# Optimization experiments

Hardware: AMD Instinct MI355X
Metric: run time of the kernel (lower is better)

## Reference

```python
import jax, jax.numpy as jnp
import numpy as np
from jax import lax

B, C, H, W = 4, 4, 64, 64
NREF = 16
DECAY = 0.8
MAX_DELAY = 24
WET_MIX, FEEDBACK, ROOM = 0.3, 0.4, 0.5  # module defaults (static Python floats)
HEADS = 4  # min(4, channels)


def _conv2d(x, w, b, pad, groups=1):
    y = lax.conv_general_dilated(x, w, (1, 1), [(pad, pad), (pad, pad)],
                                 dimension_numbers=('NCHW', 'OIHW', 'NCHW'),
                                 feature_group_count=groups)
    return y if b is None else y + b[None, :, None, None]


def _fade(n, fw=4):
    f = np.ones(n, np.float32)
    f[:fw] = np.linspace(0.6, 1.0, fw)
    f[-fw:] = np.linspace(1.0, 0.6, fw)
    return jnp.asarray(f)


def _delay_line(x, delay, yf, xf):
    # torch: shifts=(int(delay*1), int(delay*2)) on dims (2,3); delay>0 so int==floor
    ys = jnp.floor(delay).astype(jnp.int32)
    xs = jnp.floor(delay * 2.0).astype(jnp.int32)
    s = jnp.roll(x, shift=(ys, xs), axis=(2, 3))
    # shifts are always nonzero here (scaled delays >= 6), so both fades apply
    return s * yf[None, None, :, None] * xf[None, None, None, :]


def setup_inputs() -> dict:
    key = jax.random.key(0)
    ks = jax.random.split(key, 16)
    n = jax.random.normal
    return {
        'x': n(ks[0], (B, C, H, W), jnp.float32),
        'reflection_weights': n(ks[1], (NREF,), jnp.float32) * 0.1,
        'reflection_delays': jax.random.randint(ks[2], (NREF,), 1, MAX_DELAY).astype(jnp.float32),
        'diffusion_strength': n(ks[3], (NREF,), jnp.float32) * 0.2,
        'spatial_w': n(ks[4], (2 * C, C, 3, 3), jnp.float32) * 0.1,
        'spatial_b': jnp.zeros((2 * C,), jnp.float32),
        'feedback_w': n(ks[5], (C, C, 3, 3), jnp.float32) * 0.1,
        'feedback_b': jnp.zeros((C,), jnp.float32),
        'damp1_w': n(ks[6], (C // 2, C, 1, 1), jnp.float32) * 0.3,
        'damp1_b': jnp.zeros((C // 2,), jnp.float32),
        'damp2_w': n(ks[7], (C, C // 2, 1, 1), jnp.float32) * 0.3,
        'damp2_b': jnp.zeros((C,), jnp.float32),
        'attn_in_w': n(ks[8], (3 * C, C), jnp.float32) * 0.3,
        'attn_in_b': jnp.zeros((3 * C,), jnp.float32),
        'attn_out_w': n(ks[9], (C, C), jnp.float32) * 0.3,
        'attn_out_b': jnp.zeros((C,), jnp.float32),
        'out_w': n(ks[10], (C, 3 * C, 1, 1), jnp.float32) * 0.2,
        'out_b': jnp.zeros((C,), jnp.float32),
    }


def reference(x, reflection_weights, reflection_delays, diffusion_strength,
              spatial_w, spatial_b, feedback_w, feedback_b,
              damp1_w, damp1_b, damp2_w, damp2_b,
              attn_in_w, attn_in_b, attn_out_w, attn_out_b, out_w, out_b):
    b, c, h, w = x.shape
    rsf = 8.0 / NREF  # reflection_scale_factor = 0.5
    scaled_delays = reflection_delays * ROOM * 12.0 * rsf
    wet = jnp.zeros_like(x)
    fb = x * 0.1
    spatial_features = _conv2d(x, spatial_w, spatial_b, 1)
    yf, xf = _fade(h), _fade(w)
    feedback_scale = 1.0 + rsf * 0.5
    for i in range(NREF):
        delay = scaled_delays[i]
        weight = jax.nn.sigmoid(reflection_weights[i]) * (DECAY ** i) * (1.0 + FEEDBACK * feedback_scale)
        r = _delay_line(fb, delay, yf, xf)
        r = _conv2d(r, feedback_w, feedback_b, 1)
        damping = jax.nn.sigmoid(
            _conv2d(jax.nn.silu(_conv2d(r, damp1_w, damp1_b, 0)), damp2_w, damp2_b, 0))
        r = r * damping
        wet = wet + r * weight * (4.0 * rsf)
        fb = fb + r * (FEEDBACK * 1.2 * rsf)
        if FEEDBACK > 0.3 and i > 0:
            prev = _delay_line(fb, delay * 0.5, yf, xf)
            fb = fb + prev * (FEEDBACK * 0.4 * rsf)
    # spatial self-attention over flattened pixels (embed=4, 4 heads, head_dim=1)
    S = h * w
    hd = c // HEADS
    wf = wet.reshape(b, c, S).transpose(0, 2, 1)  # [b, S, c]
    qkv = wf @ attn_in_w.T + attn_in_b
    q, k, v = jnp.split(qkv, 3, axis=-1)
    def split_heads(t):
        return t.reshape(b, S, HEADS, hd).transpose(0, 2, 1, 3)  # [b, H, S, hd]
    q, k, v = split_heads(q), split_heads(k), split_heads(v)
    scores = jnp.einsum('bhqd,bhkd->bhqk', q, k) / jnp.sqrt(jnp.float32(hd))
    attn = jax.nn.softmax(scores, axis=-1)
    o = jnp.einsum('bhqk,bhkd->bhqd', attn, v).transpose(0, 2, 1, 3).reshape(b, S, c)
    o = o @ attn_out_w.T + attn_out_b
    wet = o.transpose(0, 2, 1).reshape(b, c, h, w)
    # ROOM=0.5 > 0.3 -> box blur, kernel = max(3, int(0.5*3*0.5)) = 3
    kb = 3
    blur_k = jnp.ones((c, 1, kb, kb), jnp.float32) / (kb * kb)
    wet = _conv2d(wet, blur_k, None, kb // 2, groups=c)
    # FEEDBACK=0.4 > 0.2 -> edge enhancement
    ek = jnp.array([[-1., -1., -1.], [-1., 8., -1.], [-1., -1., -1.]], jnp.float32)
    edge_k = jnp.tile(ek[None, None], (c, 1, 1, 1))
    edge = _conv2d(wet, edge_k, None, 1, groups=c)
    wet = wet + edge * (FEEDBACK * 0.2 * rsf)
    # ROOM=0.5 <= 0.8 -> no contrast adjustment
    combined = jnp.concatenate([spatial_features, wet], axis=1)
    processed = _conv2d(combined, out_w, out_b, 0)
    return x * (1.0 - WET_MIX) + processed * WET_MIX
```

## Files before the change

### kernel.cpp

```cpp
#include <hip/hip_runtime.h>

#define LOG2E 1.4426950408889634f
#define RNB 32

typedef float v2f __attribute__((ext_vector_type(2)));

__device__ __forceinline__ float fsig(float z) {
    return __builtin_amdgcn_rcpf(1.0f + exp2f(-z * LOG2E));
}

__device__ __forceinline__ float4 ld_fb(const unsigned long long* p) {
    unsigned long long a = __hip_atomic_load(p,     __ATOMIC_RELAXED, __HIP_MEMORY_SCOPE_AGENT);
    unsigned long long b = __hip_atomic_load(p + 1, __ATOMIC_RELAXED, __HIP_MEMORY_SCOPE_AGENT);
    float2 lo = __builtin_bit_cast(float2, a);
    float2 hi = __builtin_bit_cast(float2, b);
    return make_float4(lo.x, lo.y, hi.x, hi.y);
}

__device__ __forceinline__ void st_fb(unsigned long long* p, float4 v) {
    __hip_atomic_store(p,     __builtin_bit_cast(unsigned long long, make_float2(v.x, v.y)),
                       __ATOMIC_RELAXED, __HIP_MEMORY_SCOPE_AGENT);
    __hip_atomic_store(p + 1, __builtin_bit_cast(unsigned long long, make_float2(v.z, v.w)),
                       __ATOMIC_RELAXED, __HIP_MEMORY_SCOPE_AGENT);
}

__global__ __launch_bounds__(256) void bar_init(unsigned* cnt) {
    for (int j = threadIdx.x; j < 1024; j += 256) cnt[j] = 0u;
}

__device__ __forceinline__ void conv_damp_l(
    const float4* __restrict__ src, int yq, int xq, int ys, int xs,
    const float* fe, const float4 wr[9][4],
    const float4 d1w0, const float4 d1w1, const float2 d1b, const float4 d2p[4],
    float rv[4])
{
    float r[4] = { d2p[0].w, d2p[1].w, d2p[2].w, d2p[3].w };
    #pragma unroll
    for (int a = 0; a < 3; ++a) {
        int yy = yq - 1 + a;
        float fy = fe[yy + 1];
        const float4* rowp = src + (((yy - ys) & 63) << 6);
        #pragma unroll
        for (int qq = 0; qq < 3; ++qq) {
            int xt = xq - 1 + qq;
            float f = fy * fe[xt + 1];
            float4 v = rowp[(xt - xs) & 63];
            float s0 = v.x * f, s1 = v.y * f, s2 = v.z * f, s3 = v.w * f;
            #pragma unroll
            for (int co = 0; co < 4; ++co) {
                float4 w = wr[a * 3 + qq][co];
                r[co] = fmaf(w.x, s0, fmaf(w.y, s1, fmaf(w.z, s2, fmaf(w.w, s3, r[co]))));
            }
        }
    }
    float z0 = fmaf(d1w0.x, r[0], fmaf(d1w0.y, r[1], fmaf(d1w0.z, r[2], fmaf(d1w0.w, r[3], d1b.x))));
    float z1 = fmaf(d1w1.x, r[0], fmaf(d1w1.y, r[1], fmaf(d1w1.z, r[2], fmaf(d1w1.w, r[3], d1b.y))));
    float h0 = z0 * fsig(z0);
    float h1 = z1 * fsig(z1);
    #pragma unroll
    for (int c = 0; c < 4; ++c) {
        float dm = fsig(fmaf(d2p[c].x, h0, fmaf(d2p[c].y, h1, d2p[c].z)));
        rv[c] = r[c] * dm;
    }
}

__global__ __launch_bounds__(512) void reverb_mb(
    const float* __restrict__ x, const float* __restrict__ rw, const float* __restrict__ dl,
    const float* __restrict__ fbw, const float* __restrict__ fbb,
    const float* __restrict__ d1wg, const float* __restrict__ d1bg,
    const float* __restrict__ d2wg, const float* __restrict__ d2bg,
    unsigned long long* __restrict__ GA, unsigned long long* __restrict__ GB,
    unsigned* __restrict__ cnt, float4* __restrict__ ws_wet)
{
    __shared__ float4 fbL[4096];
    __shared__ float fe[66];
    __shared__ float4 wvsL[36];
    __shared__ float s_rw[16], s_dl[16];
    __shared__ float4 s_mlp[7];

    const int tid = threadIdx.x;
    const int b   = blockIdx.x >> 3;
    const int blk = blockIdx.x & 7;

    if (tid < 66) {
        float f = 0.0f;
        if (tid >= 1 && tid <= 64) {
            int j = tid - 1;
            f = 1.0f;
            if (j < 4) f = 0.6f + (0.4f / 3.0f) * j;
            else if (j >= 60) f = 0.6f + (0.4f / 3.0f) * (63 - j);
        }
        fe[tid] = f;
    }
    if (tid >= 128 && tid < 164) {
        int t2 = tid - 128, n = t2 >> 2, co = t2 & 3;
        wvsL[t2] = make_float4(fbw[(co * 4 + 0) * 9 + n], fbw[(co * 4 + 1) * 9 + n],
                               fbw[(co * 4 + 2) * 9 + n], fbw[(co * 4 + 3) * 9 + n]);
    }
    if (tid >= 192 && tid < 208) s_rw[tid - 192] = rw[tid - 192];
    if (tid >= 256 && tid < 272) s_dl[tid - 256] = dl[tid - 256];
    if (tid == 320) {
        s_mlp[0] = make_float4(d1wg[0], d1wg[1], d1wg[2], d1wg[3]);
        s_mlp[1] = make_float4(d1wg[4], d1wg[5], d1wg[6], d1wg[7]);
        s_mlp[2] = make_float4(d1bg[0], d1bg[1], 0.0f, 0.0f);
        for (int c = 0; c < 4; ++c)
            s_mlp[3 + c] = make_float4(d2wg[c * 2], d2wg[c * 2 + 1], d2bg[c], fbb[c]);
    }
    for (int s = tid; s < 4096; s += 512) {
        float4 v;
        v.x = 0.1f * x[((b * 4 + 0) << 12) + s];
        v.y = 0.1f * x[((b * 4 + 1) << 12) + s];
        v.z = 0.1f * x[((b * 4 + 2) << 12) + s];
        v.w = 0.1f * x[((b * 4 + 3) << 12) + s];
        fbL[s] = v;
    }
    __syncthreads();

    float4 wr[9][4];
    #pragma unroll
    for (int n = 0; n < 9; ++n)
        #pragma unroll
        for (int co = 0; co < 4; ++co) wr[n][co] = wvsL[n * 4 + co];
    const float4 d1w0 = s_mlp[0], d1w1 = s_mlp[1];
    const float2 d1b = make_float2(s_mlp[2].x, s_mlp[2].y);
    float4 d2p[4] = { s_mlp[3], s_mlp[4], s_mlp[5], s_mlp[6] };

    const int ly = tid >> 6;
    const int y0 = (blk << 3) + ly;
    const int xx = tid & 63;
    float4 fbv = fbL[(y0 << 6) + xx];

    unsigned long long* Ab = GA + (b << 13);
    unsigned long long* Bb = GB + (b << 13);
    unsigned* cb = cnt + b * 240;

    float acc0 = 0.0f, acc1 = 0.0f, acc2 = 0.0f, acc3 = 0.0f;
    float decay = 1.0f;
    #pragma unroll 1
    for (int i = 0; i < 16; ++i) {
        float d = s_dl[i];
        int ys  = ((int)(3.0f * d)) & 63;
        int xs  = ((int)(6.0f * d)) & 63;
        float wgt = fsig(s_rw[i]) * decay * 3.0f;

        float rv[4];
        conv_damp_l(fbL, y0, xx, ys, xs, fe, wr, d1w0, d1w1, d1b, d2p, rv);
        acc0 = fmaf(rv[0], wgt, acc0);
        acc1 = fmaf(rv[1], wgt, acc1);
        acc2 = fmaf(rv[2], wgt, acc2);
        acc3 = fmaf(rv[3], wgt, acc3);
        float4 g = make_float4(fbv.x + 0.24f * rv[0], fbv.y + 0.24f * rv[1],
                               fbv.z + 0.24f * rv[2], fbv.w + 0.24f * rv[3]);
        if (i == 15) break;

        unsigned long long* G = (i & 1) ? Bb : Ab;
        st_fb(G + (((y0 << 6) + xx) << 1), g);

        __syncthreads();
        if (tid == 0) {
            if (__hip_atomic_fetch_add(&cb[i * 16], 1u, __ATOMIC_RELAXED,
                                       __HIP_MEMORY_SCOPE_AGENT) + 1u < 8u) {
                while (__hip_atomic_load(&cb[i * 16], __ATOMIC_RELAXED,
                                         __HIP_MEMORY_SCOPE_AGENT) < 8u)
                    __builtin_amdgcn_s_sleep(1);
            }
        }
        __syncthreads();

        int ys2 = ((int)(1.5f * d)) & 63;
        int xs2 = ((int)(3.0f * d)) & 63;
        float dn = s_dl[i + 1];
        int ysn = ((int)(3.0f * dn)) & 63;

        if (i > 0) {
            int yr = (y0 - ys2) & 63, xr = (xx - xs2) & 63;
            float4 g2 = ld_fb(G + (((yr << 6) + xr) << 1));
            float f = 0.08f * fe[y0 + 1] * fe[xx + 1];
            fbv = make_float4(fmaf(f, g2.x, g.x), fmaf(f, g2.y, g.y),
                              fmaf(f, g2.z, g.z), fmaf(f, g2.w, g.w));
        } else {
            fbv = g;
        }

        #pragma unroll
        for (int rpt = 0; rpt < 2; ++rpt) {
            int idx = tid + (rpt << 9);
            if (idx < 640) {
                int j  = idx >> 6, xc = idx & 63;
                int rr = ((blk << 3) - 1 + j - ysn) & 63;
                float4 g1 = ld_fb(G + (((rr << 6) + xc) << 1));
                float4 nv = g1;
                if (i > 0) {
                    int r2 = (rr - ys2) & 63, x2 = (xc - xs2) & 63;
                    float4 g2 = ld_fb(G + (((r2 << 6) + x2) << 1));
                    float f = 0.08f * fe[rr + 1] * fe[xc + 1];
                    nv = make_float4(fmaf(f, g2.x, g1.x), fmaf(f, g2.y, g1.y),
                                     fmaf(f, g2.z, g1.z), fmaf(f, g2.w, g1.w));
                }
                fbL[(rr << 6) + xc] = nv;
            }
        }
        __syncthreads();
        decay *= 0.8f;
    }

    ws_wet[(b << 12) + (y0 << 6) + xx] = make_float4(acc0, acc1, acc2, acc3);
}

__global__ __launch_bounds__(512) void attn_kernel(
    const float4* __restrict__ wet, const float* __restrict__ aiw,
    const float* __restrict__ aib, float* __restrict__ o_out)
{
    __shared__ float ksf[4096];
    __shared__ float vsf[4096];
    __shared__ float redmx[8], redmn[8];
    __shared__ float2 part[2048];

    const int tid = threadIdx.x;
    const int bid = blockIdx.x;
    const int b  = bid >> 7;
    const int h  = (bid >> 5) & 3;
    const int qc = bid & 31;

    float wq[4], wk[4], wv[4];
    #pragma unroll
    for (int c = 0; c < 4; ++c) {
        wq[c] = aiw[h * 4 + c];
        wk[c] = aiw[(4 + h) * 4 + c];
        wv[c] = aiw[(8 + h) * 4 + c];
    }
    const float bq = aib[h], bk = aib[4 + h], bv = aib[8 + h];

    float lmax = -1e30f, lmin = 1e30f;
    for (int s = tid; s < 4096; s += 512) {
        float4 w4 = wet[(b << 12) + s];
        float k = wk[0] * w4.x + wk[1] * w4.y + wk[2] * w4.z + wk[3] * w4.w + bk;
        float v = wv[0] * w4.x + wv[1] * w4.y + wv[2] * w4.z + wv[3] * w4.w + bv;
        ksf[s] = k; vsf[s] = v;
        lmax = fmaxf(lmax, k); lmin = fminf(lmin, k);
    }
    #pragma unroll
    for (int off = 32; off > 0; off >>= 1) {
        lmax = fmaxf(lmax, __shfl_xor(lmax, off));
        lmin = fminf(lmin, __shfl_xor(lmin, off));
    }
    if ((tid & 63) == 0) { redmx[tid >> 6] = lmax; redmn[tid >> 6] = lmin; }
    __syncthreads();
    float kmax = redmx[0], kmin = redmn[0];
    #pragma unroll
    for (int w = 1; w < 8; ++w) { kmax = fmaxf(kmax, redmx[w]); kmin = fminf(kmin, redmn[w]); }

    const int rs = tid & 31;
    const int kg = tid >> 5;
    v2f qL2[4], nmL2[4];
    #pragma unroll
    for (int rr = 0; rr < 4; ++rr) {
        int row = (qc << 7) + (rs << 2) + rr;
        float4 w4 = wet[(b << 12) + row];
        float q = wq[0] * w4.x + wq[1] * w4.y + wq[2] * w4.z + wq[3] * w4.w + bq;
        float m = (q >= 0.0f) ? q * kmax : q * kmin;
        float qL = q * LOG2E, mL = m * LOG2E;
        qL2[rr] = (v2f){qL, qL}; nmL2[rr] = (v2f){-mL, -mL};
    }

    const v2f* ks2 = (const v2f*)ksf;
    const v2f* vs2 = (const v2f*)vsf;
    v2f den2[4], num2[4];
    #pragma unroll
    for (int rr = 0; rr < 4; ++rr) { den2[rr] = (v2f){0.f, 0.f}; num2[rr] = (v2f){0.f, 0.f}; }

    const int j0 = kg << 6;
    #pragma unroll 4
    for (int j = j0 * 2; j < j0 * 2 + 128; ++j) {
        v2f kk = ks2[j];
        v2f vv = vs2[j];
        #pragma unroll
        for (int rr = 0; rr < 4; ++rr) {
            v2f arg = __builtin_elementwise_fma(qL2[rr], kk, nmL2[rr]);
            v2f e;
            e.x = __builtin_amdgcn_exp2f(arg.x);
            e.y = __builtin_amdgcn_exp2f(arg.y);
            den2[rr] += e;
            num2[rr] = __builtin_elementwise_fma(e, vv, num2[rr]);
        }
    }
    #pragma unroll
    for (int rr = 0; rr < 4; ++rr)
        part[(kg << 7) + (rs << 2) + rr] =
            make_float2(den2[rr].x + den2[rr].y, num2[rr].x + num2[rr].y);
    __syncthreads();
    if (tid < 128) {
        float dd = 0.0f, nn = 0.0f;
        #pragma unroll
        for (int g = 0; g < 16; ++g) {
            float2 p = part[(g << 7) + tid];
            dd += p.x; nn += p.y;
        }
        int row = (qc << 7) + tid;
        o_out[((b << 12) + row) * 4 + h] = nn * __builtin_amdgcn_rcpf(dd);
    }
}

__global__ __launch_bounds__(256) void projblur_kernel(
    const float4* __restrict__ o_in, const float* __restrict__ aow,
    const float* __restrict__ aob, float* __restrict__ blur)
{
    __shared__ float wetL[4096];
    const int tid = threadIdx.x;
    const int bc = blockIdx.x;
    const int b = bc >> 2, c = bc & 3;
    const float w0 = aow[c * 4], w1 = aow[c * 4 + 1], w2 = aow[c * 4 + 2], w3 = aow[c * 4 + 3];
    const float bb = aob[c];
    for (int s = tid; s < 4096; s += 256) {
        float4 o = o_in[(b << 12) + s];
        wetL[s] = w0 * o.x + w1 * o.y + w2 * o.z + w3 * o.w + bb;
    }
    __syncthreads();
    for (int s = tid; s < 4096; s += 256) {
        int y = s >> 6, x = s & 63;
        float acc = 0.0f;
        for (int dy = -1; dy <= 1; ++dy) {
            int yy = y + dy; if (yy < 0 || yy > 63) continue;
            for (int dx = -1; dx <= 1; ++dx) {
                int xx = x + dx; if (xx < 0 || xx > 63) continue;
                acc += wetL[yy * 64 + xx];
            }
        }
        blur[(bc << 12) + s] = acc * (1.0f / 9.0f);
    }
}

__global__ __launch_bounds__(256) void final_kernel(
    const float* __restrict__ x, const float* __restrict__ sw, const float* __restrict__ sb,
    const float* __restrict__ ow, const float* __restrict__ ob,
    const float* __restrict__ blur, float* __restrict__ out)
{
    __shared__ float s_sw[288], s_ow[48], s_sb[8], s_ob[4];
    int tid = threadIdx.x;
    for (int j = tid; j < 288; j += 256) s_sw[j] = sw[j];
    if (tid < 48) s_ow[tid] = ow[tid];
    if (tid < 8) s_sb[tid] = sb[tid];
    if (tid < 4) s_ob[tid] = ob[tid];
    __syncthreads();

    int t = blockIdx.x * 256 + tid;
    int b = t >> 12, s = t & 4095;
    int y = s >> 6, xx0 = s & 63;

    float spat[8];
    #pragma unroll
    for (int co = 0; co < 8; ++co) spat[co] = s_sb[co];
    for (int dy = -1; dy <= 1; ++dy) {
        int yy = y + dy;
        if (yy < 0 || yy > 63) continue;
        for (int dx = -1; dx <= 1; ++dx) {
            int xc = xx0 + dx;
            if (xc < 0 || xc > 63) continue;
            int ky = dy + 1, kx = dx + 1;
            #pragma unroll
            for (int ci = 0; ci < 4; ++ci) {
                float xv = x[((b * 4 + ci) << 12) + yy * 64 + xc];
                #pragma unroll
                for (int co = 0; co < 8; ++co)
                    spat[co] += s_sw[((co * 4 + ci) * 3 + ky) * 3 + kx] * xv;
            }
        }
    }

    float wetF[4];
    #pragma unroll
    for (int c = 0; c < 4; ++c) {
        const float* pl = blur + ((b * 4 + c) << 12);
        float center = pl[s];
        float sum9 = 0.0f;
        for (int dy = -1; dy <= 1; ++dy) {
            int yy = y + dy;
            if (yy < 0 || yy > 63) continue;
            for (int dx = -1; dx <= 1; ++dx) {
                int xc = xx0 + dx;
                if (xc < 0 || xc > 63) continue;
                sum9 += pl[yy * 64 + xc];
            }
        }
        float edge = 9.0f * center - sum9;
        wetF[c] = center + 0.04f * edge;
    }

    #pragma unroll
    for (int co = 0; co < 4; ++co) {
        float p = s_ob[co];
        #pragma unroll
        for (int j = 0; j < 8; ++j) p += s_ow[co * 12 + j] * spat[j];
        #pragma unroll
        for (int c = 0; c < 4; ++c) p += s_ow[co * 12 + 8 + c] * wetF[c];
        float xc = x[((b * 4 + co) << 12) + s];
        out[((b * 4 + co) << 12) + s] = 0.7f * xc + 0.3f * p;
    }
}

extern "C" void kernel_launch(void* const* d_in, const int* in_sizes, int n_in,
                              void* d_out, int out_size, void* d_ws, size_t ws_size,
                              hipStream_t stream)
{
    (void)in_sizes; (void)n_in; (void)out_size; (void)ws_size;
    const float* x    = (const float*)d_in[0];
    const float* rw   = (const float*)d_in[1];
    const float* dl   = (const float*)d_in[2];
    const float* sw   = (const float*)d_in[4];
    const float* sb   = (const float*)d_in[5];
    const float* fbw  = (const float*)d_in[6];
    const float* fbb  = (const float*)d_in[7];
    const float* d1w  = (const float*)d_in[8];
    const float* d1b  = (const float*)d_in[9];
    const float* d2w  = (const float*)d_in[10];
    const float* d2b  = (const float*)d_in[11];
    const float* aiw  = (const float*)d_in[12];
    const float* aib  = (const float*)d_in[13];
    const float* aow  = (const float*)d_in[14];
    const float* aob  = (const float*)d_in[15];
    const float* ow   = (const float*)d_in[16];
    const float* ob   = (const float*)d_in[17];
    float* out = (float*)d_out;

    float* ws_wet  = (float*)d_ws;
    float* GA      = ws_wet + 65536;
    float* GB      = GA + 65536;
    unsigned* cnt  = (unsigned*)(GB + 65536);
    float* ws_o    = GA;
    float* ws_blur = GB;

    bar_init<<<1, 256, 0, stream>>>(cnt);
    reverb_mb<<<RNB, 512, 0, stream>>>(x, rw, dl, fbw, fbb, d1w, d1b, d2w, d2b,
                                       (unsigned long long*)GA, (unsigned long long*)GB,
                                       cnt, (float4*)ws_wet);
    attn_kernel<<<512, 512, 0, stream>>>((const float4*)ws_wet, aiw, aib, ws_o);
    projblur_kernel<<<16, 256, 0, stream>>>((const float4*)ws_o, aow, aob, ws_blur);
    final_kernel<<<64, 256, 0, stream>>>(x, sw, sb, ow, ob, ws_blur, out);
}
```

Before: 186.6 us.

## Replace counter barrier with per-block epoch flags and split projblur into bands

The inter-block barrier in the reverb kernel changes from one atomic counter per iteration, which thread 0 increments and spins on, to per-block epoch flags. Each block publishes its iteration number and then polls the minimum of the 8 flags for its batch, which removes the atomic RMW and one __syncthreads. Separately, projblur is split into 4 row bands per (b,c) with a halo, giving 64 blocks instead of 16 for more parallelism. The cost is that every thread now spins on global loads, and the halo rows are recomputed by neighbouring bands.

After: 188.8 us. About the same (+1.2%).

```diff
diff --git a/kernel.cpp b/kernel.cpp
--- a/kernel.cpp
+++ b/kernel.cpp
@@ -132,7 +132,7 @@
 
     unsigned long long* Ab = GA + (b << 13);
     unsigned long long* Bb = GB + (b << 13);
-    unsigned* cb = cnt + b * 240;
+    unsigned* flg = cnt + b * 16;
 
     float acc0 = 0.0f, acc1 = 0.0f, acc2 = 0.0f, acc3 = 0.0f;
     float decay = 1.0f;
@@ -157,15 +157,23 @@
         st_fb(G + (((y0 << 6) + xx) << 1), g);
 
         __syncthreads();
-        if (tid == 0) {
-            if (__hip_atomic_fetch_add(&cb[i * 16], 1u, __ATOMIC_RELAXED,
-                                       __HIP_MEMORY_SCOPE_AGENT) + 1u < 8u) {
-                while (__hip_atomic_load(&cb[i * 16], __ATOMIC_RELAXED,
-                                         __HIP_MEMORY_SCOPE_AGENT) < 8u)
-                    __builtin_amdgcn_s_sleep(1);
-            }
-        }
-        __syncthreads();
+        if (tid == 0)
+            __hip_atomic_store(&flg[blk], (unsigned)(i + 1),
+                               __ATOMIC_RELAXED, __HIP_MEMORY_SCOPE_AGENT);
+        {
+            const unsigned tgt = (unsigned)(i + 1);
+            for (;;) {
+                unsigned mn = 0xFFFFFFFFu;
+                #pragma unroll
+                for (int k = 0; k < 8; ++k) {
+                    unsigned fv = __hip_atomic_load(&flg[k], __ATOMIC_RELAXED,
+                                                    __HIP_MEMORY_SCOPE_AGENT);
+                    mn = (fv < mn) ? fv : mn;
+                }
+                if (mn >= tgt) break;
+                __builtin_amdgcn_s_sleep(1);
+            }
+        }
 
         int ys2 = ((int)(1.5f * d)) & 63;
         int xs2 = ((int)(3.0f * d)) & 63;
@@ -305,28 +313,39 @@
     const float4* __restrict__ o_in, const float* __restrict__ aow,
     const float* __restrict__ aob, float* __restrict__ blur)
 {
-    __shared__ float wetL[4096];
-    const int tid = threadIdx.x;
-    const int bc = blockIdx.x;
+    __shared__ float wetL[18 * 64];
+    const int tid  = threadIdx.x;
+    const int bc   = blockIdx.x >> 2;
+    const int band = blockIdx.x & 3;
     const int b = bc >> 2, c = bc & 3;
+    const int y0 = band << 4;
     const float w0 = aow[c * 4], w1 = aow[c * 4 + 1], w2 = aow[c * 4 + 2], w3 = aow[c * 4 + 3];
     const float bb = aob[c];
-    for (int s = tid; s < 4096; s += 256) {
-        float4 o = o_in[(b << 12) + s];
-        wetL[s] = w0 * o.x + w1 * o.y + w2 * o.z + w3 * o.w + bb;
+
+    {
+        const int xx = tid & 63;
+        for (int lr = tid >> 6; lr < 18; lr += 4) {
+            int gy = y0 - 1 + lr;
+            if (gy >= 0 && gy < 64) {
+                float4 o = o_in[(b << 12) + (gy << 6) + xx];
+                wetL[lr * 64 + xx] = w0 * o.x + w1 * o.y + w2 * o.z + w3 * o.w + bb;
+            }
+        }
     }
     __syncthreads();
-    for (int s = tid; s < 4096; s += 256) {
-        int y = s >> 6, x = s & 63;
+    for (int s = tid; s < 1024; s += 256) {
+        int ly = s >> 6, x = s & 63;
+        int gy = y0 + ly;
         float acc = 0.0f;
         for (int dy = -1; dy <= 1; ++dy) {
-            int yy = y + dy; if (yy < 0 || yy > 63) continue;
+            int yy = gy + dy; if (yy < 0 || yy > 63) continue;
+            int lr = yy - y0 + 1;
             for (int dx = -1; dx <= 1; ++dx) {
-                int xx = x + dx; if (xx < 0 || xx > 63) continue;
-                acc += wetL[yy * 64 + xx];
-            }
-        }
-        blur[(bc << 12) + s] = acc * (1.0f / 9.0f);
+                int xc = x + dx; if (xc < 0 || xc > 63) continue;
+                acc += wetL[lr * 64 + xc];
+            }
+        }
+        blur[(bc << 12) + (gy << 6) + x] = acc * (1.0f / 9.0f);
     }
 }
 
@@ -434,6 +453,6 @@
                                        (unsigned long long*)GA, (unsigned long long*)GB,
                                        cnt, (float4*)ws_wet);
     attn_kernel<<<512, 512, 0, stream>>>((const float4*)ws_wet, aiw, aib, ws_o);
-    projblur_kernel<<<16, 256, 0, stream>>>((const float4*)ws_o, aow, aob, ws_blur);
+    projblur_kernel<<<64, 256, 0, stream>>>((const float4*)ws_o, aow, aob, ws_blur);
     final_kernel<<<64, 256, 0, stream>>>(x, sw, sb, ow, ob, ws_blur, out);
 }
```

## Fuse projection, blur and final conv into one banded tail kernel; lighten grid barrier

Applied to the files above, without the earlier changes.

Merges the attention out-projection plus box-blur kernel with the final spatial-conv and output kernel. Each block handles a 4-row band and recomputes halo rows of projected wet and blur in shared memory, which removes one launch and the global blur round trip. It also changes the inter-block barrier in the reverb loop: one lane per wavefront now spins on the counter instead of thread 0 spinning between two __syncthreads. That drops one block-wide sync per iteration, but it relies on wavefront-level ordering and a compiler-only memory fence.

New measurement: 184.4 us. Within noise of the previous version (-1.2%).

```diff
diff --git a/kernel.cpp b/kernel.cpp
--- a/kernel.cpp
+++ b/kernel.cpp
@@ -157,15 +157,15 @@
         st_fb(G + (((y0 << 6) + xx) << 1), g);
 
         __syncthreads();
-        if (tid == 0) {
-            if (__hip_atomic_fetch_add(&cb[i * 16], 1u, __ATOMIC_RELAXED,
-                                       __HIP_MEMORY_SCOPE_AGENT) + 1u < 8u) {
-                while (__hip_atomic_load(&cb[i * 16], __ATOMIC_RELAXED,
-                                         __HIP_MEMORY_SCOPE_AGENT) < 8u)
-                    __builtin_amdgcn_s_sleep(1);
-            }
-        }
-        __syncthreads();
+        if (tid == 0)
+            __hip_atomic_fetch_add(&cb[i * 16], 1u, __ATOMIC_RELAXED,
+                                   __HIP_MEMORY_SCOPE_AGENT);
+        if ((tid & 63) == 0) {
+            while (__hip_atomic_load(&cb[i * 16], __ATOMIC_RELAXED,
+                                     __HIP_MEMORY_SCOPE_AGENT) < 8u)
+                __builtin_amdgcn_s_sleep(1);
+        }
+        asm volatile("" ::: "memory");
 
         int ys2 = ((int)(1.5f * d)) & 63;
         int xs2 = ((int)(3.0f * d)) & 63;
@@ -301,100 +301,126 @@
     }
 }
 
-__global__ __launch_bounds__(256) void projblur_kernel(
+__global__ __launch_bounds__(256) void tail_kernel(
     const float4* __restrict__ o_in, const float* __restrict__ aow,
-    const float* __restrict__ aob, float* __restrict__ blur)
+    const float* __restrict__ aob, const float* __restrict__ x,
+    const float* __restrict__ sw, const float* __restrict__ sb,
+    const float* __restrict__ ow, const float* __restrict__ ob,
+    float* __restrict__ out)
 {
-    __shared__ float wetL[4096];
-    const int tid = threadIdx.x;
-    const int bc = blockIdx.x;
-    const int b = bc >> 2, c = bc & 3;
-    const float w0 = aow[c * 4], w1 = aow[c * 4 + 1], w2 = aow[c * 4 + 2], w3 = aow[c * 4 + 3];
-    const float bb = aob[c];
-    for (int s = tid; s < 4096; s += 256) {
-        float4 o = o_in[(b << 12) + s];
-        wetL[s] = w0 * o.x + w1 * o.y + w2 * o.z + w3 * o.w + bb;
-    }
-    __syncthreads();
-    for (int s = tid; s < 4096; s += 256) {
-        int y = s >> 6, x = s & 63;
-        float acc = 0.0f;
-        for (int dy = -1; dy <= 1; ++dy) {
-            int yy = y + dy; if (yy < 0 || yy > 63) continue;
-            for (int dx = -1; dx <= 1; ++dx) {
-                int xx = x + dx; if (xx < 0 || xx > 63) continue;
-                acc += wetL[yy * 64 + xx];
-            }
-        }
-        blur[(bc << 12) + s] = acc * (1.0f / 9.0f);
-    }
-}
-
-__global__ __launch_bounds__(256) void final_kernel(
-    const float* __restrict__ x, const float* __restrict__ sw, const float* __restrict__ sb,
-    const float* __restrict__ ow, const float* __restrict__ ob,
-    const float* __restrict__ blur, float* __restrict__ out)
-{
+    __shared__ float wetp[4][8][64];
+    __shared__ float blurL[4][6][64];
+    __shared__ float xL[4][6][64];
     __shared__ float s_sw[288], s_ow[48], s_sb[8], s_ob[4];
-    int tid = threadIdx.x;
+
+    const int tid  = threadIdx.x;
+    const int b    = blockIdx.x >> 4;
+    const int band = blockIdx.x & 15;
+    const int y0   = band << 2;
+
+    float pw[4][4], pb[4];
+    #pragma unroll
+    for (int c = 0; c < 4; ++c) {
+        #pragma unroll
+        for (int h = 0; h < 4; ++h) pw[c][h] = aow[c * 4 + h];
+        pb[c] = aob[c];
+    }
+
     for (int j = tid; j < 288; j += 256) s_sw[j] = sw[j];
     if (tid < 48) s_ow[tid] = ow[tid];
-    if (tid < 8) s_sb[tid] = sb[tid];
-    if (tid < 4) s_ob[tid] = ob[tid];
+    if (tid < 8)  s_sb[tid] = sb[tid];
+    if (tid < 4)  s_ob[tid] = ob[tid];
+
+    for (int s = tid; s < 512; s += 256) {
+        int lr = s >> 6, xx = s & 63;
+        int gy = y0 - 2 + lr;
+        float4 o = make_float4(0.f, 0.f, 0.f, 0.f);
+        if (gy >= 0 && gy < 64) o = o_in[(b << 12) + (gy << 6) + xx];
+        #pragma unroll
+        for (int c = 0; c < 4; ++c)
+            wetp[c][lr][xx] = (gy >= 0 && gy < 64)
+                ? pw[c][0]*o.x + pw[c][1]*o.y + pw[c][2]*o.z + pw[c][3]*o.w + pb[c]
+                : 0.0f;
+    }
+    for (int s = tid; s < 1536; s += 256) {
+        int c = s / 384, rm = s - c * 384;
+        int r = rm >> 6, xx = rm & 63;
+        int gy = y0 - 1 + r;
+        float v = 0.f;
+        if (gy >= 0 && gy < 64) v = x[((b * 4 + c) << 12) + (gy << 6) + xx];
+        xL[c][r][xx] = v;
+    }
     __syncthreads();
 
-    int t = blockIdx.x * 256 + tid;
-    int b = t >> 12, s = t & 4095;
-    int y = s >> 6, xx0 = s & 63;
-
-    float spat[8];
-    #pragma unroll
-    for (int co = 0; co < 8; ++co) spat[co] = s_sb[co];
-    for (int dy = -1; dy <= 1; ++dy) {
-        int yy = y + dy;
-        if (yy < 0 || yy > 63) continue;
-        for (int dx = -1; dx <= 1; ++dx) {
-            int xc = xx0 + dx;
-            if (xc < 0 || xc > 63) continue;
-            int ky = dy + 1, kx = dx + 1;
-            #pragma unroll
-            for (int ci = 0; ci < 4; ++ci) {
-                float xv = x[((b * 4 + ci) << 12) + yy * 64 + xc];
+    for (int s = tid; s < 1536; s += 256) {
+        int c = s / 384, rm = s - c * 384;
+        int r = rm >> 6, xx = rm & 63;
+        int gy = y0 - 1 + r;
+        float acc = 0.f;
+        if (gy >= 0 && gy < 64) {
+            #pragma unroll
+            for (int dy = 0; dy < 3; ++dy) {
                 #pragma unroll
-                for (int co = 0; co < 8; ++co)
-                    spat[co] += s_sw[((co * 4 + ci) * 3 + ky) * 3 + kx] * xv;
+                for (int dx = -1; dx <= 1; ++dx) {
+                    int xc = xx + dx;
+                    if (xc >= 0 && xc <= 63) acc += wetp[c][r + dy][xc];
+                }
             }
         }
-    }
-
-    float wetF[4];
-    #pragma unroll
-    for (int c = 0; c < 4; ++c) {
-        const float* pl = blur + ((b * 4 + c) << 12);
-        float center = pl[s];
-        float sum9 = 0.0f;
-        for (int dy = -1; dy <= 1; ++dy) {
-            int yy = y + dy;
-            if (yy < 0 || yy > 63) continue;
+        blurL[c][r][xx] = acc * (1.0f / 9.0f);
+    }
+    __syncthreads();
+
+    {
+        const int lyq = tid >> 6, xx = tid & 63;
+        const int gy = y0 + lyq;
+
+        float spat[8];
+        #pragma unroll
+        for (int co = 0; co < 8; ++co) spat[co] = s_sb[co];
+        #pragma unroll
+        for (int dy = 0; dy < 3; ++dy) {
+            #pragma unroll
             for (int dx = -1; dx <= 1; ++dx) {
-                int xc = xx0 + dx;
+                int xc = xx + dx;
                 if (xc < 0 || xc > 63) continue;
-                sum9 += pl[yy * 64 + xc];
+                int kx = dx + 1;
+                #pragma unroll
+                for (int ci = 0; ci < 4; ++ci) {
+                    float xv = xL[ci][lyq + dy][xc];
+                    #pragma unroll
+                    for (int co = 0; co < 8; ++co)
+                        spat[co] += s_sw[((co * 4 + ci) * 3 + dy) * 3 + kx] * xv;
+                }
             }
         }
-        float edge = 9.0f * center - sum9;
-        wetF[c] = center + 0.04f * edge;
-    }
-
-    #pragma unroll
-    for (int co = 0; co < 4; ++co) {
-        float p = s_ob[co];
-        #pragma unroll
-        for (int j = 0; j < 8; ++j) p += s_ow[co * 12 + j] * spat[j];
-        #pragma unroll
-        for (int c = 0; c < 4; ++c) p += s_ow[co * 12 + 8 + c] * wetF[c];
-        float xc = x[((b * 4 + co) << 12) + s];
-        out[((b * 4 + co) << 12) + s] = 0.7f * xc + 0.3f * p;
+
+        float wetF[4];
+        #pragma unroll
+        for (int c = 0; c < 4; ++c) {
+            float center = blurL[c][lyq + 1][xx];
+            float sum9 = 0.f;
+            #pragma unroll
+            for (int dy = 0; dy < 3; ++dy) {
+                #pragma unroll
+                for (int dx = -1; dx <= 1; ++dx) {
+                    int xc = xx + dx;
+                    if (xc >= 0 && xc <= 63) sum9 += blurL[c][lyq + dy][xc];
+                }
+            }
+            wetF[c] = center + 0.04f * (9.0f * center - sum9);
+        }
+
+        #pragma unroll
+        for (int co = 0; co < 4; ++co) {
+            float p = s_ob[co];
+            #pragma unroll
+            for (int j = 0; j < 8; ++j) p += s_ow[co * 12 + j] * spat[j];
+            #pragma unroll
+            for (int c = 0; c < 4; ++c) p += s_ow[co * 12 + 8 + c] * wetF[c];
+            float xc = xL[co][lyq + 1][xx];
+            out[((b * 4 + co) << 12) + (gy << 6) + xx] = 0.7f * xc + 0.3f * p;
+        }
     }
 }
 
@@ -427,13 +453,12 @@
     float* GB      = GA + 65536;
     unsigned* cnt  = (unsigned*)(GB + 65536);
     float* ws_o    = GA;
-    float* ws_blur = GB;
 
     bar_init<<<1, 256, 0, stream>>>(cnt);
     reverb_mb<<<RNB, 512, 0, stream>>>(x, rw, dl, fbw, fbb, d1w, d1b, d2w, d2b,
                                        (unsigned long long*)GA, (unsigned long long*)GB,
                                        cnt, (float4*)ws_wet);
     attn_kernel<<<512, 512, 0, stream>>>((const float4*)ws_wet, aiw, aib, ws_o);
-    projblur_kernel<<<16, 256, 0, stream>>>((const float4*)ws_o, aow, aob, ws_blur);
-    final_kernel<<<64, 256, 0, stream>>>(x, sw, sb, ow, ob, ws_blur, out);
-}
+    tail_kernel<<<64, 256, 0, stream>>>((const float4*)ws_o, aow, aob, x,
+                                        sw, sb, ow, ob, out);
+}
```
